# Performance work log

Hardware: AMD Instinct MI355X
Metric: run time of the kernel (lower is better)

Reference implementation:

```python
import jax, jax.numpy as jnp
import numpy as np

N_NODES = 50000
N_EDGES = 1600000
D_IN = 128
D_HID = 128
D_OUT = 128


def setup_inputs() -> dict:
    key = jax.random.key(0)
    k = jax.random.split(key, 6)
    feat = jax.random.normal(k[0], (N_NODES, D_IN), dtype=jnp.float32)
    W1 = jax.random.normal(k[1], (D_IN, D_HID), dtype=jnp.float32) * (1.0 / np.sqrt(D_IN))
    b1 = jnp.zeros((D_HID,), dtype=jnp.float32)
    W2 = jax.random.normal(k[2], (D_HID, D_OUT), dtype=jnp.float32) * (1.0 / np.sqrt(D_HID))
    b2 = jnp.zeros((D_OUT,), dtype=jnp.float32)
    src = jax.random.randint(k[3], (N_EDGES,), 0, N_NODES, dtype=jnp.int32)
    dst = jax.random.randint(k[4], (N_EDGES,), 0, N_NODES, dtype=jnp.int32)
    return {"feat": feat, "W1": W1, "b1": b1, "W2": W2, "b2": b2, "src": src, "dst": dst}


def _graph_conv(h, W, b, src, dst, norm_src, norm_dst, n_nodes):
    # DGL GraphConv, norm='both': h_src * out_deg^-1/2 -> sum over edges -> * in_deg^-1/2 -> W, +b
    h = h * norm_src[:, None]
    agg = jax.ops.segment_sum(h[src], dst, num_segments=n_nodes)
    agg = agg * norm_dst[:, None]
    return agg @ W + b


def reference(feat, W1, b1, W2, b2, src, dst):
    n = feat.shape[0]
    # dgl.add_self_loop: append (i, i) for every node
    loop = jnp.arange(n, dtype=src.dtype)
    src = jnp.concatenate([src, loop])
    dst = jnp.concatenate([dst, loop])
    ones = jnp.ones(src.shape[0], dtype=feat.dtype)
    out_deg = jax.ops.segment_sum(ones, src, num_segments=n)  # >= 1 due to self-loops
    in_deg = jax.ops.segment_sum(ones, dst, num_segments=n)
    norm_src = jax.lax.rsqrt(out_deg)
    norm_dst = jax.lax.rsqrt(in_deg)
    h = _graph_conv(feat, W1, b1, src, dst, norm_src, norm_dst, n)
    h = jax.nn.relu(h)
    h = _graph_conv(h, W2, b2, src, dst, norm_src, norm_dst, n)
    return h[None, :, :]  # unsqueeze(0) -> [1, N, out_features]
```

## Files before the change

kernel.cpp:

```cpp
#include <hip/hip_runtime.h>

#define D 128
#define RANGES 4
#define CHUNKS 64
#define BINS_MAX 12512


__device__ __forceinline__ unsigned short f2bf(float x) {
  unsigned u = __float_as_uint(x);
  u += 0x7fffu + ((u >> 16) & 1u);
  return (unsigned short)(u >> 16);
}
#define BF_LO(u) __uint_as_float((u) << 16)
#define BF_HI(u) __uint_as_float((u) & 0xffff0000u)


__global__ __launch_bounds__(1024)
void hist_kernel(const int* __restrict__ keys, int* __restrict__ part,
                 int E, int N, int binsR, int chunkE)
{
  __shared__ int hist[BINS_MAX];
  const int b = blockIdx.x;
  const int r = b & (RANGES - 1);
  const int k = b >> 2;
  const int lo = r * binsR;
  const int hi = min(N, lo + binsR);
  const int nb = hi - lo;
  for (int i = threadIdx.x; i < nb; i += 1024) hist[i] = 0;
  __syncthreads();
  const int e0 = k * chunkE;
  const int e1 = min(E, e0 + chunkE);
  for (int e = e0 + threadIdx.x; e < e1; e += 1024) {
    int v = keys[e];
    if (v >= lo && v < hi) atomicAdd(&hist[v - lo], 1);
  }
  __syncthreads();
  for (int i = threadIdx.x; i < nb; i += 1024) part[(size_t)k * N + lo + i] = hist[i];
}

__global__ void reduce_kernel(const int* __restrict__ psrc, int* __restrict__ pdst,
                              int* __restrict__ deg_in, float* __restrict__ nsrc,
                              float* __restrict__ ndst, int N)
{
  int bin = blockIdx.x * blockDim.x + threadIdx.x;
  if (bin >= N) return;
  int runs = 0, rund = 0;
  for (int k = 0; k < CHUNKS; ++k) {
    runs += psrc[(size_t)k * N + bin];
    int vd = pdst[(size_t)k * N + bin];
    pdst[(size_t)k * N + bin] = rund;
    rund += vd;
  }
  deg_in[bin] = rund;
  nsrc[bin] = rsqrtf((float)runs + 1.0f);
  ndst[bin] = rsqrtf((float)rund + 1.0f);
}


__global__ __launch_bounds__(1024)
void scan1_kernel(const int* __restrict__ din, int* __restrict__ roff,
                  int* __restrict__ bsum, int N)
{
  __shared__ int wsum[16];
  const int t = threadIdx.x, lane = t & 63, wid = t >> 6;
  const int i = blockIdx.x * 1024 + t;
  int v = (i < N) ? din[i] : 0;
  int x = v;
  #pragma unroll
  for (int off = 1; off < 64; off <<= 1) {
    int u = __shfl_up(x, off);
    if (lane >= off) x += u;
  }
  if (lane == 63) wsum[wid] = x;
  __syncthreads();
  if (wid == 0) {
    int y = (lane < 16) ? wsum[lane] : 0;
    int z = y;
    #pragma unroll
    for (int off = 1; off < 16; off <<= 1) {
      int u = __shfl_up(z, off);
      if (lane >= off) z += u;
    }
    if (lane < 16) wsum[lane] = z - y;
    if (lane == 15) bsum[blockIdx.x] = z;
  }
  __syncthreads();
  if (i < N) roff[i] = wsum[wid] + (x - v);
}

__global__ void scan2_kernel(int* __restrict__ bsum, int* __restrict__ roffN, int nb)
{
  const int t = threadIdx.x;
  int v = (t < nb) ? bsum[t] : 0;
  int x = v;
  #pragma unroll
  for (int off = 1; off < 64; off <<= 1) {
    int u = __shfl_up(x, off);
    if (t >= off) x += u;
  }
  if (t < nb) bsum[t] = x - v;
  if (t == 63) *roffN = x;
}

__global__ __launch_bounds__(1024)
void scan3_kernel(int* __restrict__ roff, const int* __restrict__ bsum, int N)
{
  const int i = blockIdx.x * 1024 + threadIdx.x;
  if (i < N) roff[i] += bsum[i >> 10];
}


__global__ __launch_bounds__(1024)
void scatter_kernel(const int* __restrict__ src, const int* __restrict__ dst,
                    const int* __restrict__ pdst, const int* __restrict__ roff,
                    int* __restrict__ eout, int E, int N, int binsR, int chunkE)
{
  __shared__ int cur[BINS_MAX];
  const int b = blockIdx.x;
  const int r = b & (RANGES - 1);
  const int k = b >> 2;
  const int lo = r * binsR;
  const int hi = min(N, lo + binsR);
  const int nb = hi - lo;
  for (int i = threadIdx.x; i < nb; i += 1024)
    cur[i] = roff[lo + i] + pdst[(size_t)k * N + lo + i];
  __syncthreads();
  const int e0 = k * chunkE;
  const int e1 = min(E, e0 + chunkE);
  for (int e = e0 + threadIdx.x; e < e1; e += 1024) {
    int d = dst[e];
    if (d >= lo && d < hi) eout[atomicAdd(&cur[d - lo], 1)] = src[e];
  }
}


__global__ __launch_bounds__(256)
void convert_kernel(const float* __restrict__ f, unsigned* __restrict__ fb, int n4)
{
  const int i = blockIdx.x * blockDim.x + threadIdx.x;
  if (i < n4) {
    float4 v = ((const float4*)f)[i];
    uint2 o;
    o.x = (unsigned)f2bf(v.x) | ((unsigned)f2bf(v.y) << 16);
    o.y = (unsigned)f2bf(v.z) | ((unsigned)f2bf(v.w) << 16);
    ((uint2*)fb)[i] = o;
  }
}


template<bool SCALE>
__global__ __launch_bounds__(256)
void gather_bf_kernel(const unsigned* __restrict__ fb, const int* __restrict__ eidx,
                      const int* __restrict__ roff, const float* __restrict__ nsrc,
                      const float* __restrict__ ndst, float* __restrict__ out, int N)
{
  const int wid = threadIdx.x >> 6;
  const int lane = threadIdx.x & 63;
  const int node = blockIdx.x * 4 + wid;
  if (node >= N) return;
  unsigned sv = fb[(size_t)node * 64 + lane];
  float sn = SCALE ? nsrc[node] : 1.0f;
  float2 acc = make_float2(BF_LO(sv) * sn, BF_HI(sv) * sn);
  const int beg = roff[node], end = roff[node + 1];
  for (int e0 = beg; e0 < end; e0 += 64) {
    const int cnt = min(64, end - e0);
    int id = (lane < cnt) ? eidx[e0 + lane] : 0;
    int j = 0;
    for (; j + 8 <= cnt; j += 8) {
      int s0 = __shfl(id, j + 0), s1 = __shfl(id, j + 1);
      int s2 = __shfl(id, j + 2), s3 = __shfl(id, j + 3);
      int s4 = __shfl(id, j + 4), s5 = __shfl(id, j + 5);
      int s6 = __shfl(id, j + 6), s7 = __shfl(id, j + 7);
      unsigned u0 = fb[(size_t)s0 * 64 + lane];
      unsigned u1 = fb[(size_t)s1 * 64 + lane];
      unsigned u2 = fb[(size_t)s2 * 64 + lane];
      unsigned u3 = fb[(size_t)s3 * 64 + lane];
      unsigned u4 = fb[(size_t)s4 * 64 + lane];
      unsigned u5 = fb[(size_t)s5 * 64 + lane];
      unsigned u6 = fb[(size_t)s6 * 64 + lane];
      unsigned u7 = fb[(size_t)s7 * 64 + lane];
      float n0 = SCALE ? nsrc[s0] : 1.0f, n1 = SCALE ? nsrc[s1] : 1.0f;
      float n2 = SCALE ? nsrc[s2] : 1.0f, n3 = SCALE ? nsrc[s3] : 1.0f;
      float n4 = SCALE ? nsrc[s4] : 1.0f, n5 = SCALE ? nsrc[s5] : 1.0f;
      float n6 = SCALE ? nsrc[s6] : 1.0f, n7 = SCALE ? nsrc[s7] : 1.0f;
      acc.x += BF_LO(u0) * n0; acc.y += BF_HI(u0) * n0;
      acc.x += BF_LO(u1) * n1; acc.y += BF_HI(u1) * n1;
      acc.x += BF_LO(u2) * n2; acc.y += BF_HI(u2) * n2;
      acc.x += BF_LO(u3) * n3; acc.y += BF_HI(u3) * n3;
      acc.x += BF_LO(u4) * n4; acc.y += BF_HI(u4) * n4;
      acc.x += BF_LO(u5) * n5; acc.y += BF_HI(u5) * n5;
      acc.x += BF_LO(u6) * n6; acc.y += BF_HI(u6) * n6;
      acc.x += BF_LO(u7) * n7; acc.y += BF_HI(u7) * n7;
    }
    for (; j < cnt; ++j) {
      int s = __shfl(id, j);
      unsigned u = fb[(size_t)s * 64 + lane];
      float n = SCALE ? nsrc[s] : 1.0f;
      acc.x += BF_LO(u) * n; acc.y += BF_HI(u) * n;
    }
  }
  float nd = ndst[node];
  acc.x *= nd; acc.y *= nd;
  *(float2*)(out + (size_t)node * D + lane * 2) = acc;
}


template<bool RELU_SCALE, bool BF_OUT>
__global__ __launch_bounds__(256)
void gemm128(const float* __restrict__ A, const float* __restrict__ W,
             const float* __restrict__ bias, const float* __restrict__ nsrc,
             void* __restrict__ Cv, int N)
{
  __shared__ float As[64][36];
  __shared__ float Bs[32][128];
  const int t = threadIdx.x;
  const int tx = t & 15;
  const int ty = t >> 4;
  const int r0 = blockIdx.x * 64;
  float acc[4][8];
  #pragma unroll
  for (int j = 0; j < 4; ++j)
    #pragma unroll
    for (int cc = 0; cc < 8; ++cc) acc[j][cc] = 0.f;

  for (int kc = 0; kc < D; kc += 32) {
    __syncthreads();
    #pragma unroll
    for (int m = 0; m < 2; ++m) {
      int q = t * 2 + m;
      int row = q >> 3;
      int fc = q & 7;
      int gr = r0 + row; if (gr > N - 1) gr = N - 1;
      float4 v = *(const float4*)(A + (size_t)gr * D + kc + fc * 4);
      *(float4*)(&As[row][fc * 4]) = v;
    }
    #pragma unroll
    for (int m = 0; m < 4; ++m) {
      int q = t + 256 * m;
      int kk = q >> 5;
      int fc = q & 31;
      float4 v = *(const float4*)(W + (size_t)(kc + kk) * D + fc * 4);
      *(float4*)(&Bs[kk][fc * 4]) = v;
    }
    __syncthreads();
    #pragma unroll
    for (int k = 0; k < 32; ++k) {
      float a0 = As[ty * 4 + 0][k];
      float a1 = As[ty * 4 + 1][k];
      float a2 = As[ty * 4 + 2][k];
      float a3 = As[ty * 4 + 3][k];
      float4 bv0 = *(const float4*)(&Bs[k][tx * 4]);
      float4 bv1 = *(const float4*)(&Bs[k][64 + tx * 4]);
      float bb[8] = {bv0.x, bv0.y, bv0.z, bv0.w, bv1.x, bv1.y, bv1.z, bv1.w};
      #pragma unroll
      for (int cc = 0; cc < 8; ++cc) {
        acc[0][cc] += a0 * bb[cc];
        acc[1][cc] += a1 * bb[cc];
        acc[2][cc] += a2 * bb[cc];
        acc[3][cc] += a3 * bb[cc];
      }
    }
  }

  float4 bb0 = *(const float4*)(bias + tx * 4);
  float4 bb1 = *(const float4*)(bias + 64 + tx * 4);
  float bb[8] = {bb0.x, bb0.y, bb0.z, bb0.w, bb1.x, bb1.y, bb1.z, bb1.w};
  #pragma unroll
  for (int j = 0; j < 4; ++j) {
    int gr = r0 + ty * 4 + j;
    if (gr < N) {
      float s = RELU_SCALE ? nsrc[gr] : 1.0f;
      float o[8];
      #pragma unroll
      for (int cc = 0; cc < 8; ++cc) {
        float v = acc[j][cc] + bb[cc];
        if (RELU_SCALE) v = fmaxf(v, 0.f) * s;
        o[cc] = v;
      }
      if (BF_OUT) {
        unsigned short* Cb = (unsigned short*)Cv;
        ushort4 w0, w1;
        w0.x = f2bf(o[0]); w0.y = f2bf(o[1]); w0.z = f2bf(o[2]); w0.w = f2bf(o[3]);
        w1.x = f2bf(o[4]); w1.y = f2bf(o[5]); w1.z = f2bf(o[6]); w1.w = f2bf(o[7]);
        *(ushort4*)(Cb + (size_t)gr * D + tx * 4) = w0;
        *(ushort4*)(Cb + (size_t)gr * D + 64 + tx * 4) = w1;
      } else {
        float* C = (float*)Cv;
        *(float4*)(C + (size_t)gr * D + tx * 4) = make_float4(o[0], o[1], o[2], o[3]);
        *(float4*)(C + (size_t)gr * D + 64 + tx * 4) = make_float4(o[4], o[5], o[6], o[7]);
      }
    }
  }
}


extern "C" void kernel_launch(void* const* d_in, const int* in_sizes, int n_in,
                              void* d_out, int out_size, void* d_ws, size_t ws_size,
                              hipStream_t stream) {
  const float* feat = (const float*)d_in[0];
  const float* W1   = (const float*)d_in[1];
  const float* b1   = (const float*)d_in[2];
  const float* W2   = (const float*)d_in[3];
  const float* b2   = (const float*)d_in[4];
  const int*   src  = (const int*)d_in[5];
  const int*   dst  = (const int*)d_in[6];
  const int N = in_sizes[0] / D;
  const int E = in_sizes[5];
  float* out = (float*)d_out;

  const int binsR = (N + RANGES - 1) / RANGES;
  const int chunkE = (((E + CHUNKS - 1) / CHUNKS) + 3) & ~3;

  auto align256 = [](size_t x) { return (x + 255) & ~(size_t)255; };
  char* p = (char*)d_ws;
  int*   esrc    = (int*)p;   p += align256((size_t)E * 4);
  char*  big     = p;         p += 2 * align256((size_t)CHUNKS * N * 4);
  int*   deg_in  = (int*)p;   p += align256((size_t)N * 4);
  int*   row_off = (int*)p;   p += align256((size_t)(N + 1) * 4);
  float* nsrc    = (float*)p; p += align256((size_t)N * 4);
  float* ndst    = (float*)p; p += align256((size_t)N * 4);
  int*   bsum    = (int*)p;   p += 256;
  int*      psrc   = (int*)big;
  int*      pdst   = (int*)(big + align256((size_t)CHUNKS * N * 4));
  unsigned* featbf = (unsigned*)psrc;
  unsigned* h1bf   = (unsigned*)pdst;

  const int nblk = (N + 1023) / 1024;

  hist_kernel<<<RANGES * CHUNKS, 1024, 0, stream>>>(src, psrc, E, N, binsR, chunkE);
  hist_kernel<<<RANGES * CHUNKS, 1024, 0, stream>>>(dst, pdst, E, N, binsR, chunkE);
  reduce_kernel<<<(N + 255) / 256, 256, 0, stream>>>(psrc, pdst, deg_in, nsrc, ndst, N);
  convert_kernel<<<(N * D / 4 + 255) / 256, 256, 0, stream>>>(feat, featbf, N * D / 4);
  scan1_kernel<<<nblk, 1024, 0, stream>>>(deg_in, row_off, bsum, N);
  scan2_kernel<<<1, 64, 0, stream>>>(bsum, row_off + N, nblk);
  scan3_kernel<<<nblk, 1024, 0, stream>>>(row_off, bsum, N);
  scatter_kernel<<<RANGES * CHUNKS, 1024, 0, stream>>>(src, dst, pdst, row_off, esrc, E, N, binsR, chunkE);

  gather_bf_kernel<true><<<(N + 3) / 4, 256, 0, stream>>>(featbf, esrc, row_off, nsrc, ndst, out, N);
  gemm128<true, true><<<(N + 63) / 64, 256, 0, stream>>>(out, W1, b1, nsrc, h1bf, N);
  gather_bf_kernel<false><<<(N + 3) / 4, 256, 0, stream>>>(h1bf, esrc, row_off, nsrc, ndst, out, N);
  gemm128<false, false><<<(N + 63) / 64, 256, 0, stream>>>(out, W2, b2, nsrc, out, N);
}
```

Baseline: 315.7 us.

## Pre-scale bf16 features, use u16 partial histograms, half-wave gather with 8-byte loads

The source-norm scaling is folded into the feature-to-bf16 conversion, so the first gather no longer loads nsrc once per edge. The gather now splits each wave into two 32-lane halves that each handle a different edge using 8-byte row loads, then combines the halves with a cross-half shuffle. Per-chunk histogram partials are stored as 16-bit counts, which halves the partial-count traffic in the hist, reduce and scatter kernels. The workspace is re-aliased so these buffers share space. The risk is that u16 partial counts overflow if a chunk's per-node counts or per-node prefix exceed 65535, and the extra shuffle reduction adds a little per-node overhead.

Result: no change. 314.4 us (-0.4%).

```diff
diff --git a/kernel.cpp b/kernel.cpp
--- a/kernel.cpp
+++ b/kernel.cpp
@@ -5,18 +5,20 @@
 #define CHUNKS 64
 #define BINS_MAX 12512
 
-
-__device__ __forceinline__ unsigned short f2bf(float x) {
+typedef unsigned short u16;
+
+
+__device__ __forceinline__ u16 f2bf(float x) {
   unsigned u = __float_as_uint(x);
   u += 0x7fffu + ((u >> 16) & 1u);
-  return (unsigned short)(u >> 16);
+  return (u16)(u >> 16);
 }
 #define BF_LO(u) __uint_as_float((u) << 16)
 #define BF_HI(u) __uint_as_float((u) & 0xffff0000u)
 
 
 __global__ __launch_bounds__(1024)
-void hist_kernel(const int* __restrict__ keys, int* __restrict__ part,
+void hist_kernel(const int* __restrict__ keys, u16* __restrict__ part,
                  int E, int N, int binsR, int chunkE)
 {
   __shared__ int hist[BINS_MAX];
@@ -35,10 +37,11 @@
     if (v >= lo && v < hi) atomicAdd(&hist[v - lo], 1);
   }
   __syncthreads();
-  for (int i = threadIdx.x; i < nb; i += 1024) part[(size_t)k * N + lo + i] = hist[i];
-}
-
-__global__ void reduce_kernel(const int* __restrict__ psrc, int* __restrict__ pdst,
+  for (int i = threadIdx.x; i < nb; i += 1024)
+    part[(size_t)k * N + lo + i] = (u16)hist[i];
+}
+
+__global__ void reduce_kernel(const u16* __restrict__ psrc, u16* __restrict__ pdst,
                               int* __restrict__ deg_in, float* __restrict__ nsrc,
                               float* __restrict__ ndst, int N)
 {
@@ -48,7 +51,7 @@
   for (int k = 0; k < CHUNKS; ++k) {
     runs += psrc[(size_t)k * N + bin];
     int vd = pdst[(size_t)k * N + bin];
-    pdst[(size_t)k * N + bin] = rund;
+    pdst[(size_t)k * N + bin] = (u16)rund;
     rund += vd;
   }
   deg_in[bin] = rund;
@@ -112,7 +115,7 @@
 
 __global__ __launch_bounds__(1024)
 void scatter_kernel(const int* __restrict__ src, const int* __restrict__ dst,
-                    const int* __restrict__ pdst, const int* __restrict__ roff,
+                    const u16* __restrict__ pdst, const int* __restrict__ roff,
                     int* __restrict__ eout, int E, int N, int binsR, int chunkE)
 {
   __shared__ int cur[BINS_MAX];
@@ -123,7 +126,7 @@
   const int hi = min(N, lo + binsR);
   const int nb = hi - lo;
   for (int i = threadIdx.x; i < nb; i += 1024)
-    cur[i] = roff[lo + i] + pdst[(size_t)k * N + lo + i];
+    cur[i] = roff[lo + i] + (int)pdst[(size_t)k * N + lo + i];
   __syncthreads();
   const int e0 = k * chunkE;
   const int e1 = min(E, e0 + chunkE);
@@ -135,73 +138,89 @@
 
 
 __global__ __launch_bounds__(256)
-void convert_kernel(const float* __restrict__ f, unsigned* __restrict__ fb, int n4)
+void convert_kernel(const float* __restrict__ f, const float* __restrict__ nsrc,
+                    unsigned* __restrict__ fb, int n4)
 {
   const int i = blockIdx.x * blockDim.x + threadIdx.x;
   if (i < n4) {
+    float s = nsrc[i >> 5];
     float4 v = ((const float4*)f)[i];
     uint2 o;
-    o.x = (unsigned)f2bf(v.x) | ((unsigned)f2bf(v.y) << 16);
-    o.y = (unsigned)f2bf(v.z) | ((unsigned)f2bf(v.w) << 16);
+    o.x = (unsigned)f2bf(v.x * s) | ((unsigned)f2bf(v.y * s) << 16);
+    o.y = (unsigned)f2bf(v.z * s) | ((unsigned)f2bf(v.w * s) << 16);
     ((uint2*)fb)[i] = o;
   }
 }
 
 
-template<bool SCALE>
 __global__ __launch_bounds__(256)
 void gather_bf_kernel(const unsigned* __restrict__ fb, const int* __restrict__ eidx,
-                      const int* __restrict__ roff, const float* __restrict__ nsrc,
-                      const float* __restrict__ ndst, float* __restrict__ out, int N)
+                      const int* __restrict__ roff, const float* __restrict__ ndst,
+                      float* __restrict__ out, int N)
 {
   const int wid = threadIdx.x >> 6;
   const int lane = threadIdx.x & 63;
   const int node = blockIdx.x * 4 + wid;
   if (node >= N) return;
-  unsigned sv = fb[(size_t)node * 64 + lane];
-  float sn = SCALE ? nsrc[node] : 1.0f;
-  float2 acc = make_float2(BF_LO(sv) * sn, BF_HI(sv) * sn);
+  const int h = lane >> 5;
+  const int q = lane & 31;
+  const uint2* fb2 = (const uint2*)fb;
+  float4 acc = make_float4(0.f, 0.f, 0.f, 0.f);
+  if (h == 0) {
+    uint2 u = fb2[(size_t)node * 32 + q];
+    acc.x = BF_LO(u.x); acc.y = BF_HI(u.x);
+    acc.z = BF_LO(u.y); acc.w = BF_HI(u.y);
+  }
   const int beg = roff[node], end = roff[node + 1];
   for (int e0 = beg; e0 < end; e0 += 64) {
     const int cnt = min(64, end - e0);
     int id = (lane < cnt) ? eidx[e0 + lane] : 0;
     int j = 0;
-    for (; j + 8 <= cnt; j += 8) {
-      int s0 = __shfl(id, j + 0), s1 = __shfl(id, j + 1);
-      int s2 = __shfl(id, j + 2), s3 = __shfl(id, j + 3);
-      int s4 = __shfl(id, j + 4), s5 = __shfl(id, j + 5);
-      int s6 = __shfl(id, j + 6), s7 = __shfl(id, j + 7);
-      unsigned u0 = fb[(size_t)s0 * 64 + lane];
-      unsigned u1 = fb[(size_t)s1 * 64 + lane];
-      unsigned u2 = fb[(size_t)s2 * 64 + lane];
-      unsigned u3 = fb[(size_t)s3 * 64 + lane];
-      unsigned u4 = fb[(size_t)s4 * 64 + lane];
-      unsigned u5 = fb[(size_t)s5 * 64 + lane];
-      unsigned u6 = fb[(size_t)s6 * 64 + lane];
-      unsigned u7 = fb[(size_t)s7 * 64 + lane];
-      float n0 = SCALE ? nsrc[s0] : 1.0f, n1 = SCALE ? nsrc[s1] : 1.0f;
-      float n2 = SCALE ? nsrc[s2] : 1.0f, n3 = SCALE ? nsrc[s3] : 1.0f;
-      float n4 = SCALE ? nsrc[s4] : 1.0f, n5 = SCALE ? nsrc[s5] : 1.0f;
-      float n6 = SCALE ? nsrc[s6] : 1.0f, n7 = SCALE ? nsrc[s7] : 1.0f;
-      acc.x += BF_LO(u0) * n0; acc.y += BF_HI(u0) * n0;
-      acc.x += BF_LO(u1) * n1; acc.y += BF_HI(u1) * n1;
-      acc.x += BF_LO(u2) * n2; acc.y += BF_HI(u2) * n2;
-      acc.x += BF_LO(u3) * n3; acc.y += BF_HI(u3) * n3;
-      acc.x += BF_LO(u4) * n4; acc.y += BF_HI(u4) * n4;
-      acc.x += BF_LO(u5) * n5; acc.y += BF_HI(u5) * n5;
-      acc.x += BF_LO(u6) * n6; acc.y += BF_HI(u6) * n6;
-      acc.x += BF_LO(u7) * n7; acc.y += BF_HI(u7) * n7;
-    }
-    for (; j < cnt; ++j) {
-      int s = __shfl(id, j);
-      unsigned u = fb[(size_t)s * 64 + lane];
-      float n = SCALE ? nsrc[s] : 1.0f;
-      acc.x += BF_LO(u) * n; acc.y += BF_HI(u) * n;
-    }
-  }
-  float nd = ndst[node];
-  acc.x *= nd; acc.y *= nd;
-  *(float2*)(out + (size_t)node * D + lane * 2) = acc;
+    for (; j + 16 <= cnt; j += 16) {
+      int s0 = __shfl(id, j + 0 + h);
+      int s1 = __shfl(id, j + 2 + h);
+      int s2 = __shfl(id, j + 4 + h);
+      int s3 = __shfl(id, j + 6 + h);
+      int s4 = __shfl(id, j + 8 + h);
+      int s5 = __shfl(id, j + 10 + h);
+      int s6 = __shfl(id, j + 12 + h);
+      int s7 = __shfl(id, j + 14 + h);
+      uint2 u0 = fb2[(size_t)s0 * 32 + q];
+      uint2 u1 = fb2[(size_t)s1 * 32 + q];
+      uint2 u2 = fb2[(size_t)s2 * 32 + q];
+      uint2 u3 = fb2[(size_t)s3 * 32 + q];
+      uint2 u4 = fb2[(size_t)s4 * 32 + q];
+      uint2 u5 = fb2[(size_t)s5 * 32 + q];
+      uint2 u6 = fb2[(size_t)s6 * 32 + q];
+      uint2 u7 = fb2[(size_t)s7 * 32 + q];
+      acc.x += BF_LO(u0.x); acc.y += BF_HI(u0.x); acc.z += BF_LO(u0.y); acc.w += BF_HI(u0.y);
+      acc.x += BF_LO(u1.x); acc.y += BF_HI(u1.x); acc.z += BF_LO(u1.y); acc.w += BF_HI(u1.y);
+      acc.x += BF_LO(u2.x); acc.y += BF_HI(u2.x); acc.z += BF_LO(u2.y); acc.w += BF_HI(u2.y);
+      acc.x += BF_LO(u3.x); acc.y += BF_HI(u3.x); acc.z += BF_LO(u3.y); acc.w += BF_HI(u3.y);
+      acc.x += BF_LO(u4.x); acc.y += BF_HI(u4.x); acc.z += BF_LO(u4.y); acc.w += BF_HI(u4.y);
+      acc.x += BF_LO(u5.x); acc.y += BF_HI(u5.x); acc.z += BF_LO(u5.y); acc.w += BF_HI(u5.y);
+      acc.x += BF_LO(u6.x); acc.y += BF_HI(u6.x); acc.z += BF_LO(u6.y); acc.w += BF_HI(u6.y);
+      acc.x += BF_LO(u7.x); acc.y += BF_HI(u7.x); acc.z += BF_LO(u7.y); acc.w += BF_HI(u7.y);
+    }
+    for (; j < cnt; j += 2) {
+      int ej = j + h;
+      int s = __shfl(id, ej & 63);
+      if (ej < cnt) {
+        uint2 u = fb2[(size_t)s * 32 + q];
+        acc.x += BF_LO(u.x); acc.y += BF_HI(u.x);
+        acc.z += BF_LO(u.y); acc.w += BF_HI(u.y);
+      }
+    }
+  }
+  acc.x += __shfl_xor(acc.x, 32);
+  acc.y += __shfl_xor(acc.y, 32);
+  acc.z += __shfl_xor(acc.z, 32);
+  acc.w += __shfl_xor(acc.w, 32);
+  if (h == 0) {
+    float nd = ndst[node];
+    acc.x *= nd; acc.y *= nd; acc.z *= nd; acc.w *= nd;
+    *(float4*)(out + (size_t)node * D + q * 4) = acc;
+  }
 }
 
 
@@ -278,7 +297,7 @@
         o[cc] = v;
       }
       if (BF_OUT) {
-        unsigned short* Cb = (unsigned short*)Cv;
+        u16* Cb = (u16*)Cv;
         ushort4 w0, w1;
         w0.x = f2bf(o[0]); w0.y = f2bf(o[1]); w0.z = f2bf(o[2]); w0.w = f2bf(o[3]);
         w1.x = f2bf(o[4]); w1.y = f2bf(o[5]); w1.z = f2bf(o[6]); w1.w = f2bf(o[7]);
@@ -313,31 +332,34 @@
 
   auto align256 = [](size_t x) { return (x + 255) & ~(size_t)255; };
   char* p = (char*)d_ws;
-  int*   esrc    = (int*)p;   p += align256((size_t)E * 4);
-  char*  big     = p;         p += 2 * align256((size_t)CHUNKS * N * 4);
+  char* p0 = p;  p += align256((size_t)E * 4);
+  char* p1 = p;  p += align256((size_t)N * D * 2);
+  char* p2 = p;  p += align256((size_t)N * D * 2);
   int*   deg_in  = (int*)p;   p += align256((size_t)N * 4);
   int*   row_off = (int*)p;   p += align256((size_t)(N + 1) * 4);
   float* nsrc    = (float*)p; p += align256((size_t)N * 4);
   float* ndst    = (float*)p; p += align256((size_t)N * 4);
   int*   bsum    = (int*)p;   p += 256;
-  int*      psrc   = (int*)big;
-  int*      pdst   = (int*)(big + align256((size_t)CHUNKS * N * 4));
-  unsigned* featbf = (unsigned*)psrc;
-  unsigned* h1bf   = (unsigned*)pdst;
+
+  u16*      psrc   = (u16*)p0;
+  int*      esrc   = (int*)p0;
+  u16*      pdst   = (u16*)p1;
+  u16*      h1bf   = (u16*)p1;
+  unsigned* featbf = (unsigned*)p2;
 
   const int nblk = (N + 1023) / 1024;
 
   hist_kernel<<<RANGES * CHUNKS, 1024, 0, stream>>>(src, psrc, E, N, binsR, chunkE);
   hist_kernel<<<RANGES * CHUNKS, 1024, 0, stream>>>(dst, pdst, E, N, binsR, chunkE);
   reduce_kernel<<<(N + 255) / 256, 256, 0, stream>>>(psrc, pdst, deg_in, nsrc, ndst, N);
-  convert_kernel<<<(N * D / 4 + 255) / 256, 256, 0, stream>>>(feat, featbf, N * D / 4);
+  convert_kernel<<<(N * D / 4 + 255) / 256, 256, 0, stream>>>(feat, nsrc, featbf, N * D / 4);
   scan1_kernel<<<nblk, 1024, 0, stream>>>(deg_in, row_off, bsum, N);
   scan2_kernel<<<1, 64, 0, stream>>>(bsum, row_off + N, nblk);
   scan3_kernel<<<nblk, 1024, 0, stream>>>(row_off, bsum, N);
   scatter_kernel<<<RANGES * CHUNKS, 1024, 0, stream>>>(src, dst, pdst, row_off, esrc, E, N, binsR, chunkE);
 
-  gather_bf_kernel<true><<<(N + 3) / 4, 256, 0, stream>>>(featbf, esrc, row_off, nsrc, ndst, out, N);
+  gather_bf_kernel<<<(N + 3) / 4, 256, 0, stream>>>(featbf, esrc, row_off, ndst, out, N);
   gemm128<true, true><<<(N + 63) / 64, 256, 0, stream>>>(out, W1, b1, nsrc, h1bf, N);
-  gather_bf_kernel<false><<<(N + 3) / 4, 256, 0, stream>>>(h1bf, esrc, row_off, nsrc, ndst, out, N);
+  gather_bf_kernel<<<(N + 3) / 4, 256, 0, stream>>>((const unsigned*)h1bf, esrc, row_off, ndst, out, N);
   gemm128<false, false><<<(N + 63) / 64, 256, 0, stream>>>(out, W2, b2, nsrc, out, N);
 }
```
